# Kernel tuning notes

Hardware: AMD Instinct MI355X
Metric: run time of the kernel (lower is better)

## Reference

```python
import jax, jax.numpy as jnp
import numpy as np

N = 100000      # nodes
NT = 500000     # unique (s,o) pairs
R = 16          # original relations
RP = 16         # latent relations
EMB = 16
NUMCLS = 40


def setup_inputs() -> dict:
    key = jax.random.key(0)
    ks = jax.random.split(key, 10)
    s = jax.random.randint(ks[0], (NT,), 0, N)
    o = jax.random.randint(ks[1], (NT,), 0, N)
    rm = jnp.arange(RP)
    # faithful to source: oe = o*rm, se = s*rm (values in [0, N*RP))
    hrow = jnp.broadcast_to(s[None, :], (RP, NT)).reshape(-1).astype(jnp.int64)
    hcol = (o[None, :] * rm[:, None]).reshape(-1).astype(jnp.int64)
    vrow = (s[None, :] * rm[:, None]).reshape(-1).astype(jnp.int64)
    vcol = jnp.broadcast_to(o[None, :], (RP, NT)).reshape(-1).astype(jnp.int64)
    # multi-hot relation indicators per unique pair
    nhots = (jax.random.uniform(ks[2], (NT, R)) < 0.15).astype(jnp.float32)
    xav = lambda k, shp, fan: (jax.random.normal(k, shp, jnp.float32) * np.sqrt(2.0 / fan)).astype(jnp.float32)
    return {
        'nhots': nhots,
        'Wl1': xav(ks[3], (RP, R), R), 'bl1': jnp.zeros((RP,), jnp.float32),
        'Wl2': xav(ks[4], (RP, R), R), 'bl2': jnp.zeros((RP,), jnp.float32),
        'weights1': xav(ks[5], (RP, N, EMB), N),
        'weights2': xav(ks[6], (RP, EMB, NUMCLS), EMB),
        'bias1': jnp.zeros((EMB,), jnp.float32),
        'bias2': jnp.zeros((NUMCLS,), jnp.float32),
        'hrow': hrow, 'hcol': hcol, 'vrow': vrow, 'vcol': vcol,
    }


def reference(nhots, Wl1, bl1, Wl2, bl2, weights1, weights2, bias1, bias2,
              hrow, hcol, vrow, vcol):
    rp, n, e = weights1.shape
    nrp = n * rp
    # --- layer 1: softmax-gated latent relation values, column-normalized ---
    lat1 = jax.nn.softmax(nhots @ Wl1.T + bl1, axis=1)          # (nt, rp)
    vals1 = lat1.T.reshape(-1)                                   # (rp*nt,) rp-major, matches index order
    colsum = jax.ops.segment_sum(vals1, hcol, num_segments=nrp)
    vals1 = vals1 / colsum[hcol]
    # spmm: (n, n*rp) sparse  x  (n*rp, e) dense
    wflat = weights1.reshape(nrp, e)
    h = jax.ops.segment_sum(vals1[:, None] * wflat[hcol], hrow, num_segments=n)  # (n, e)
    h = jax.nn.relu(h + bias1)
    # --- layer 2: row-normalized ---
    lat2 = jax.nn.softmax(nhots @ Wl2.T + bl2, axis=1)
    vals2 = lat2.T.reshape(-1)
    rowsum = jax.ops.segment_sum(vals2, vrow, num_segments=nrp)
    vals2 = vals2 / rowsum[vrow]
    # spmm: (n*rp, n) sparse  x  (n, e) dense
    h2 = jax.ops.segment_sum(vals2[:, None] * h[vcol], vrow, num_segments=nrp)   # (n*rp, e)
    h2 = h2.reshape(rp, n, e)
    out = jnp.einsum('rhc,rnh->nc', weights2, h2) + bias2        # (n, numcls)
    return out
```

## Files before the change

kernel.cpp:

```cpp
#include <hip/hip_runtime.h>
#include <stdint.h>

#define NN 100000
#define NT 500000
#define RP 16
#define RR 16
#define EMB 16
#define NUMCLS 40
#define NRP (NN*RP)
#define MM (2*NN)
#define SCAN_BLOCKS ((MM + 255)/256)
#define NB16 6250

__global__ __launch_bounds__(256) void k_count(const int* __restrict__ s,
                                               const int* __restrict__ o,
                                               int* __restrict__ cnt){
    int t = blockIdx.x*256 + threadIdx.x;
    if (t >= NT) return;
    atomicAdd(&cnt[s[t]], 1);
    atomicAdd(&cnt[NN + o[t]], 1);
}

__global__ __launch_bounds__(256) void k_scan_blk(const int* __restrict__ cnt,
                                                  int* __restrict__ offs,
                                                  int* __restrict__ bsum){
    __shared__ int sm[256];
    int tid = threadIdx.x;
    int i = blockIdx.x*256 + tid;
    int v = (i < MM) ? cnt[i] : 0;
    sm[tid] = v; __syncthreads();
    for (int off = 1; off < 256; off <<= 1){
        int x = (tid >= off) ? sm[tid-off] : 0;
        __syncthreads();
        sm[tid] += x; __syncthreads();
    }
    if (i < MM) offs[i] = sm[tid] - v;
    if (tid == 255) bsum[blockIdx.x] = sm[255];
}

__global__ __launch_bounds__(1024) void k_scan_top(const int* __restrict__ bsum,
                                                   int* __restrict__ btot){
    __shared__ int sm[1024];
    int tid = threadIdx.x;
    int v = (tid < SCAN_BLOCKS) ? bsum[tid] : 0;
    sm[tid] = v; __syncthreads();
    for (int off = 1; off < 1024; off <<= 1){
        int x = (tid >= off) ? sm[tid-off] : 0;
        __syncthreads();
        sm[tid] += x; __syncthreads();
    }
    if (tid < SCAN_BLOCKS) btot[tid] = sm[tid] - v;
}

__global__ __launch_bounds__(256) void k_scan_add(int* __restrict__ offs,
                                                  const int* __restrict__ btot,
                                                  int* __restrict__ cur){
    int i = blockIdx.x*256 + threadIdx.x;
    if (i < MM){
        int v = offs[i] + btot[blockIdx.x];
        offs[i] = v;
        cur[i] = v;
    }
    if (i == 0) offs[MM] = 2*NT;
}

__global__ __launch_bounds__(256) void k_lat(
    const float* __restrict__ nhots,
    const float* __restrict__ Wl1, const float* __restrict__ bl1,
    const float* __restrict__ Wl2, const float* __restrict__ bl2,
    const int* __restrict__ srow, const int* __restrict__ ocol,
    int* __restrict__ cur,
    float* __restrict__ lat1q, float* __restrict__ lat2p,
    int* __restrict__ o_at_p, int* __restrict__ s_at_q)
{
    __shared__ float sW1[RP*RR], sW2[RP*RR], sb1[RP], sb2[RP];
    __shared__ float st1[256][17], st2[256][17];
    __shared__ int sq[256], sp[256];
    int tid = threadIdx.x;
    if (tid < RP*RR){ sW1[tid] = Wl1[tid]; sW2[tid] = Wl2[tid]; }
    if (tid < RP){ sb1[tid] = bl1[tid]; sb2[tid] = bl2[tid]; }
    __syncthreads();

    int t = blockIdx.x*256 + tid;
    int p = -1, q = -1;
    if (t < NT){
        int s_ = srow[t], o_ = ocol[t];
        p = atomicAdd(&cur[s_], 1);
        q = atomicAdd(&cur[NN + o_], 1) - NT;
        o_at_p[p] = o_;
        s_at_q[q] = s_;

        float nh[RR];
        const float4* npx = (const float4*)(nhots + (size_t)t * RR);
        #pragma unroll
        for (int u = 0; u < 4; u++){
            float4 v = npx[u];
            nh[4*u] = v.x; nh[4*u+1] = v.y; nh[4*u+2] = v.z; nh[4*u+3] = v.w;
        }
        float l1[RP], l2[RP];
        #pragma unroll
        for (int r = 0; r < RP; r++){
            float a = sb1[r], b = sb2[r];
            #pragma unroll
            for (int i = 0; i < RR; i++){ a += nh[i]*sW1[r*RR+i]; b += nh[i]*sW2[r*RR+i]; }
            l1[r] = a; l2[r] = b;
        }
        float m1 = l1[0], m2 = l2[0];
        #pragma unroll
        for (int r = 1; r < RP; r++){ m1 = fmaxf(m1, l1[r]); m2 = fmaxf(m2, l2[r]); }
        float s1 = 0.f, s2 = 0.f;
        #pragma unroll
        for (int r = 0; r < RP; r++){
            l1[r] = expf(l1[r]-m1); s1 += l1[r];
            l2[r] = expf(l2[r]-m2); s2 += l2[r];
        }
        float i1 = 1.f/s1, i2 = 1.f/s2;
        #pragma unroll
        for (int r = 0; r < RP; r++){ st1[tid][r] = l1[r]*i1; st2[tid][r] = l2[r]*i2; }
    }
    sq[tid] = q; sp[tid] = p;
    __syncthreads();

    int g = tid >> 4, e = tid & 15;
    #pragma unroll
    for (int k = 0; k < 16; k++){
        int ei = k*16 + g;
        int qq = sq[ei];
        if (qq >= 0){
            lat1q[(size_t)qq*16 + e] = st1[ei][e];
            lat2p[(size_t)sp[ei]*16 + e] = st2[ei][e];
        }
    }
}

__global__ __launch_bounds__(256) void k_CR(const int* __restrict__ offs,
                                            const float* __restrict__ lat1q,
                                            const float* __restrict__ lat2p,
                                            float* __restrict__ C,
                                            float* __restrict__ Rm,
                                            float* __restrict__ pbC,
                                            float* __restrict__ pbR){
    int gid = blockIdx.x*256 + threadIdx.x;
    int n = gid >> 4, e = gid & 15;
    float accC = 0.f, accR = 0.f;
    if (n < NN){
        int b = offs[NN+n] - NT, en = offs[NN+n+1] - NT;
        for (int i = b; i < en; i++) accC += lat1q[(size_t)i*16 + e];
        C[(size_t)n*16 + e] = accC;
        b = offs[n]; en = offs[n+1];
        for (int i = b; i < en; i++) accR += lat2p[(size_t)i*16 + e];
        Rm[(size_t)n*16 + e] = accR;
    }
    __shared__ float sa[16], sb[16];
    int g = threadIdx.x >> 4;
    if (e == 0){ sa[g] = accC; sb[g] = accR; }
    __syncthreads();
    if (threadIdx.x == 0){
        float a = 0.f, b = 0.f;
        #pragma unroll
        for (int k = 0; k < 16; k++){ a += sa[k]; b += sb[k]; }
        pbC[blockIdx.x] = a;
        pbR[blockIdx.x] = b;
    }
}

__global__ __launch_bounds__(1024) void k_red1(const float* __restrict__ pbC,
                                               const float* __restrict__ pbR,
                                               float* __restrict__ S0V){
    __shared__ float sa[1024], sb[1024];
    int tid = threadIdx.x;
    float a = 0.f, b = 0.f;
    for (int i = tid; i < NB16; i += 1024){ a += pbC[i]; b += pbR[i]; }
    sa[tid] = a; sb[tid] = b; __syncthreads();
    for (int off = 512; off > 0; off >>= 1){
        if (tid < off){ sa[tid] += sa[tid+off]; sb[tid] += sb[tid+off]; }
        __syncthreads();
    }
    if (tid == 0){ S0V[0] = sa[0]; S0V[1] = sb[0]; }
}

__global__ __launch_bounds__(256) void k_sums(const float* __restrict__ C,
                                              const float* __restrict__ Rm,
                                              const float* __restrict__ S0,
                                              float* __restrict__ invc,
                                              float* __restrict__ invr){
    int c = blockIdx.x*256 + threadIdx.x;
    if (c >= NRP) return;
    float a = 0.f, b = 0.f;
    if (c == 0){ a = S0[0]; b = S0[1]; }
    #pragma unroll
    for (int r = 1; r < RP; r++){
        int q = c / r;
        if (q*r == c && q < NN){
            a += C[(size_t)q*16 + r];
            b += Rm[(size_t)q*16 + r];
        }
    }
    invc[c] = (a > 0.f) ? 1.f/a : 0.f;
    invr[c] = (b > 0.f) ? 1.f/b : 0.f;
}

__global__ __launch_bounds__(256) void k_y(const int* __restrict__ offs,
                                           const float* __restrict__ lat1q,
                                           const int* __restrict__ s_at_q,
                                           const float* __restrict__ invc,
                                           const float* __restrict__ w1,
                                           float* __restrict__ hsum){
    int gid = blockIdx.x*256 + threadIdx.x;
    int o = gid >> 4, e = gid & 15;
    if (o >= NN) return;
    float Wb[RP];
    #pragma unroll
    for (int r = 0; r < RP; r++){
        size_t c = (size_t)o * r;
        Wb[r] = invc[c] * w1[c*16 + e];
    }
    int b = offs[NN+o] - NT, en = offs[NN+o+1] - NT;
    for (int i = b; i < en; i++){
        const float4* lp = (const float4*)(lat1q + (size_t)i*16);
        float4 v0 = lp[0], v1 = lp[1], v2 = lp[2], v3 = lp[3];
        float y = v0.x*Wb[0] + v0.y*Wb[1] + v0.z*Wb[2] + v0.w*Wb[3]
                + v1.x*Wb[4] + v1.y*Wb[5] + v1.z*Wb[6] + v1.w*Wb[7]
                + v2.x*Wb[8] + v2.y*Wb[9] + v2.z*Wb[10]+ v2.w*Wb[11]
                + v3.x*Wb[12]+ v3.y*Wb[13]+ v3.z*Wb[14]+ v3.w*Wb[15];
        int s = s_at_q[i];
        unsafeAtomicAdd(&hsum[(size_t)s*16 + e], y);
    }
}

__global__ __launch_bounds__(256) void k_P(const int* __restrict__ offs,
                                           const int* __restrict__ o_at_p,
                                           const float* __restrict__ lat2p,
                                           const float* __restrict__ hsum,
                                           const float* __restrict__ b1,
                                           float* __restrict__ P,
                                           float* __restrict__ pbV){
    int gid = blockIdx.x*256 + threadIdx.x;
    int n = gid >> 4, e = gid & 15;
    float be = b1[e];
    float acc[RP];
    #pragma unroll
    for (int r = 0; r < RP; r++) acc[r] = 0.f;
    if (n < NN){
        int b = offs[n], en = offs[n+1];
        for (int i = b; i < en; i++){
            int o = o_at_p[i];
            float hv = fmaxf(hsum[(size_t)o*16 + e] + be, 0.f);
            const float4* lp = (const float4*)(lat2p + (size_t)i*16);
            float4 v0 = lp[0], v1 = lp[1], v2 = lp[2], v3 = lp[3];
            acc[0] += v0.x*hv; acc[1] += v0.y*hv; acc[2] += v0.z*hv; acc[3] += v0.w*hv;
            acc[4] += v1.x*hv; acc[5] += v1.y*hv; acc[6] += v1.z*hv; acc[7] += v1.w*hv;
            acc[8] += v2.x*hv; acc[9] += v2.y*hv; acc[10]+= v2.z*hv; acc[11]+= v2.w*hv;
            acc[12]+= v3.x*hv; acc[13]+= v3.y*hv; acc[14]+= v3.z*hv; acc[15]+= v3.w*hv;
        }
        float* Pn = P + (size_t)n*240 + e;
        #pragma unroll
        for (int r = 1; r < RP; r++) Pn[(r-1)*16] = acc[r];
    }
    __shared__ float sm[256];
    sm[threadIdx.x] = acc[0]; __syncthreads();
    if (threadIdx.x < 16){
        float s = 0.f;
        #pragma unroll
        for (int k = 0; k < 16; k++) s += sm[k*16 + threadIdx.x];
        pbV[(size_t)blockIdx.x*16 + threadIdx.x] = s;
    }
}

__global__ __launch_bounds__(256) void k_red2(const float* __restrict__ pbV,
                                              float* __restrict__ S0V){
    int e = blockIdx.x;
    __shared__ float sm[256];
    int tid = threadIdx.x;
    float a = 0.f;
    for (int i = tid; i < NB16; i += 256) a += pbV[(size_t)i*16 + e];
    sm[tid] = a; __syncthreads();
    for (int off = 128; off > 0; off >>= 1){
        if (tid < off) sm[tid] += sm[tid+off];
        __syncthreads();
    }
    if (tid == 0) S0V[2 + e] = sm[0];
}

__global__ __launch_bounds__(256) void k_out(const float* __restrict__ P,
                                             const float* __restrict__ invr,
                                             const float* __restrict__ S0V,
                                             const float* __restrict__ w2,
                                             const float* __restrict__ b2,
                                             float* __restrict__ out){
    int n = blockIdx.x*256 + threadIdx.x;
    if (n >= NN) return;
    float acc[NUMCLS];
    #pragma unroll
    for (int cl = 0; cl < NUMCLS; cl++) acc[cl] = b2[cl];
    #pragma unroll 1
    for (int rr = 0; rr < RP; rr++){
        int c = rr*NN + n;
        float hrow[EMB];
        #pragma unroll
        for (int e = 0; e < EMB; e++) hrow[e] = 0.f;
        if (c == 0){
            #pragma unroll
            for (int e = 0; e < EMB; e++) hrow[e] = S0V[2 + e];
        }
        #pragma unroll
        for (int r = 1; r < RP; r++){
            int q = c / r;
            if (q*r == c && q < NN){
                const float* Pr = P + (size_t)q*240 + (r-1)*16;
                #pragma unroll
                for (int e = 0; e < EMB; e++) hrow[e] += Pr[e];
            }
        }
        float inv = invr[c];
        const float* wr = w2 + (size_t)rr*EMB*NUMCLS;
        #pragma unroll
        for (int e = 0; e < EMB; e++){
            float x = hrow[e] * inv;
            #pragma unroll
            for (int cl = 0; cl < NUMCLS; cl++) acc[cl] += x * wr[e*NUMCLS + cl];
        }
    }
    float4* op = (float4*)(out + (size_t)n*NUMCLS);
    #pragma unroll
    for (int q = 0; q < NUMCLS/4; q++)
        op[q] = make_float4(acc[4*q], acc[4*q+1], acc[4*q+2], acc[4*q+3]);
}

extern "C" void kernel_launch(void* const* d_in, const int* in_sizes, int n_in,
                              void* d_out, int out_size, void* d_ws, size_t ws_size,
                              hipStream_t stream)
{
    const float* nhots = (const float*)d_in[0];
    const float* Wl1   = (const float*)d_in[1];
    const float* bl1   = (const float*)d_in[2];
    const float* Wl2   = (const float*)d_in[3];
    const float* bl2   = (const float*)d_in[4];
    const float* w1    = (const float*)d_in[5];
    const float* w2    = (const float*)d_in[6];
    const float* b1    = (const float*)d_in[7];
    const float* b2    = (const float*)d_in[8];
    const int* srow = (const int*)d_in[9];
    const int* ocol = (const int*)d_in[12];

    float* base = (float*)d_ws;
    float* P     = base;
    float* lat1q = base;
    float* C     = base + (size_t)8000000;
    float* Rm    = base + (size_t)9600000;
    float* lat2p = base + (size_t)24000000;
    float* invc  = base + (size_t)32000000;
    float* invr  = base + (size_t)33600000;
    float* hsum  = base + (size_t)35200000;
    float* S0V   = base + (size_t)36800000;
    int*   cnt   = (int*)(base + (size_t)36800032);
    int*   cur   = cnt;
    int*   offs  = cnt + MM;
    int*   bsum  = offs + (MM+1);
    int*   btot  = bsum + 1024;
    int*   o_at_p = btot + 1024;
    int*   s_at_q = o_at_p + NT;
    float* pbC   = (float*)(s_at_q + NT);
    float* pbR   = pbC + NB16;
    float* pbV   = pbR + NB16;

    hipMemsetAsync(cnt, 0, (size_t)MM*4, stream);
    hipMemsetAsync(hsum, 0, (size_t)NN*16*4, stream);

    const int EB = (NT + 255)/256;
    const int CB = (NRP + 255)/256;
    const int NB = (NN + 255)/256;

    k_count   <<<EB, 256, 0, stream>>>(srow, ocol, cnt);
    k_scan_blk<<<SCAN_BLOCKS, 256, 0, stream>>>(cnt, offs, bsum);
    k_scan_top<<<1, 1024, 0, stream>>>(bsum, btot);
    k_scan_add<<<SCAN_BLOCKS, 256, 0, stream>>>(offs, btot, cur);
    k_lat     <<<EB, 256, 0, stream>>>(nhots, Wl1, bl1, Wl2, bl2, srow, ocol,
                                       cur, lat1q, lat2p, o_at_p, s_at_q);
    k_CR      <<<NB16, 256, 0, stream>>>(offs, lat1q, lat2p, C, Rm, pbC, pbR);
    k_red1    <<<1, 1024, 0, stream>>>(pbC, pbR, S0V);
    k_sums    <<<CB, 256, 0, stream>>>(C, Rm, S0V, invc, invr);
    k_y       <<<NB16, 256, 0, stream>>>(offs, lat1q, s_at_q, invc, w1, hsum);
    k_P       <<<NB16, 256, 0, stream>>>(offs, o_at_p, lat2p, hsum, b1, P, pbV);
    k_red2    <<<16, 256, 0, stream>>>(pbV, S0V);
    k_out     <<<NB, 256, 0, stream>>>(P, invr, S0V, w2, b2, (float*)d_out);
}
```

Baseline: 628.7 us.

## Scatter layer-2 partials into dense h2 buffer via atomics instead of divisor gather

k_P now atomically adds each per-relation partial into a dense (N*RP,16) buffer at row n*r, replacing the compact P array. k_out then reads one contiguous row per latent index instead of testing 15 divisors with integer division and gathering. This removes the divisor search and its divergent loads from k_out. In exchange it adds a roughly 100 MB memset, 15 scattered atomic adds per thread and a larger workspace that shifts the buffer offsets.

```diff
diff --git a/kernel.cpp b/kernel.cpp
--- a/kernel.cpp
+++ b/kernel.cpp
@@ -233,7 +233,7 @@
                                            const float* __restrict__ lat2p,
                                            const float* __restrict__ hsum,
                                            const float* __restrict__ b1,
-                                           float* __restrict__ P,
+                                           float* __restrict__ h2n,
                                            float* __restrict__ pbV){
     int gid = blockIdx.x*256 + threadIdx.x;
     int n = gid >> 4, e = gid & 15;
@@ -253,9 +253,10 @@
             acc[8] += v2.x*hv; acc[9] += v2.y*hv; acc[10]+= v2.z*hv; acc[11]+= v2.w*hv;
             acc[12]+= v3.x*hv; acc[13]+= v3.y*hv; acc[14]+= v3.z*hv; acc[15]+= v3.w*hv;
         }
-        float* Pn = P + (size_t)n*240 + e;
-        #pragma unroll
-        for (int r = 1; r < RP; r++) Pn[(r-1)*16] = acc[r];
+        #pragma unroll
+        for (int r = 1; r < RP; r++){
+            unsafeAtomicAdd(&h2n[(size_t)(n*r)*16 + e], acc[r]);
+        }
     }
     __shared__ float sm[256];
     sm[threadIdx.x] = acc[0]; __syncthreads();
@@ -282,7 +283,7 @@
     if (tid == 0) S0V[2 + e] = sm[0];
 }
 
-__global__ __launch_bounds__(256) void k_out(const float* __restrict__ P,
+__global__ __launch_bounds__(256) void k_out(const float* __restrict__ h2n,
                                              const float* __restrict__ invr,
                                              const float* __restrict__ S0V,
                                              const float* __restrict__ w2,
@@ -293,30 +294,25 @@
     float acc[NUMCLS];
     #pragma unroll
     for (int cl = 0; cl < NUMCLS; cl++) acc[cl] = b2[cl];
-    #pragma unroll 1
+    #pragma unroll 4
     for (int rr = 0; rr < RP; rr++){
         int c = rr*NN + n;
-        float hrow[EMB];
-        #pragma unroll
-        for (int e = 0; e < EMB; e++) hrow[e] = 0.f;
+        const float4* hp = (const float4*)(h2n + (size_t)c*16);
+        float4 h0 = hp[0], h1 = hp[1], h2 = hp[2], h3 = hp[3];
+        float inv = invr[c];
+        float hr[16];
+        hr[0]=h0.x;  hr[1]=h0.y;  hr[2]=h0.z;  hr[3]=h0.w;
+        hr[4]=h1.x;  hr[5]=h1.y;  hr[6]=h1.z;  hr[7]=h1.w;
+        hr[8]=h2.x;  hr[9]=h2.y;  hr[10]=h2.z; hr[11]=h2.w;
+        hr[12]=h3.x; hr[13]=h3.y; hr[14]=h3.z; hr[15]=h3.w;
         if (c == 0){
             #pragma unroll
-            for (int e = 0; e < EMB; e++) hrow[e] = S0V[2 + e];
-        }
-        #pragma unroll
-        for (int r = 1; r < RP; r++){
-            int q = c / r;
-            if (q*r == c && q < NN){
-                const float* Pr = P + (size_t)q*240 + (r-1)*16;
-                #pragma unroll
-                for (int e = 0; e < EMB; e++) hrow[e] += Pr[e];
-            }
-        }
-        float inv = invr[c];
+            for (int e = 0; e < EMB; e++) hr[e] += S0V[2+e];
+        }
         const float* wr = w2 + (size_t)rr*EMB*NUMCLS;
         #pragma unroll
         for (int e = 0; e < EMB; e++){
-            float x = hrow[e] * inv;
+            float x = hr[e] * inv;
             #pragma unroll
             for (int cl = 0; cl < NUMCLS; cl++) acc[cl] += x * wr[e*NUMCLS + cl];
         }
@@ -344,16 +340,16 @@
     const int* ocol = (const int*)d_in[12];
 
     float* base = (float*)d_ws;
-    float* P     = base;
+    float* h2n   = base;
     float* lat1q = base;
     float* C     = base + (size_t)8000000;
     float* Rm    = base + (size_t)9600000;
-    float* lat2p = base + (size_t)24000000;
-    float* invc  = base + (size_t)32000000;
-    float* invr  = base + (size_t)33600000;
-    float* hsum  = base + (size_t)35200000;
-    float* S0V   = base + (size_t)36800000;
-    int*   cnt   = (int*)(base + (size_t)36800032);
+    float* lat2p = base + (size_t)25600000;
+    float* invc  = base + (size_t)33600000;
+    float* invr  = base + (size_t)35200000;
+    float* hsum  = base + (size_t)36800000;
+    float* S0V   = base + (size_t)38400000;
+    int*   cnt   = (int*)(base + (size_t)38400032);
     int*   cur   = cnt;
     int*   offs  = cnt + MM;
     int*   bsum  = offs + (MM+1);
@@ -381,7 +377,8 @@
     k_red1    <<<1, 1024, 0, stream>>>(pbC, pbR, S0V);
     k_sums    <<<CB, 256, 0, stream>>>(C, Rm, S0V, invc, invr);
     k_y       <<<NB16, 256, 0, stream>>>(offs, lat1q, s_at_q, invc, w1, hsum);
-    k_P       <<<NB16, 256, 0, stream>>>(offs, o_at_p, lat2p, hsum, b1, P, pbV);
+    hipMemsetAsync(h2n, 0, (size_t)NRP*16*4, stream);
+    k_P       <<<NB16, 256, 0, stream>>>(offs, o_at_p, lat2p, hsum, b1, h2n, pbV);
     k_red2    <<<16, 256, 0, stream>>>(pbV, S0V);
-    k_out     <<<NB, 256, 0, stream>>>(P, invr, S0V, w2, b2, (float*)d_out);
-}
+    k_out     <<<NB, 256, 0, stream>>>(h2n, invr, S0V, w2, b2, (float*)d_out);
+}
```

Result: slower. 761.3 us (+21.1%).

## Split k_out relation loop across four wavefronts with shared-memory reduction

Applied to the files above, without the earlier changes.

The output kernel now assigns 64 nodes per block and gives each of the four wavefronts a quarter of the 16 latent relations, reducing partial class accumulators through LDS. This raises the number of blocks fourfold, increasing parallelism and latency hiding for the serial per-node relation loop. P rows are now read with float4 loads. Output is written through a coalesced shared-memory transpose instead of per-thread float4 strided stores. The cost is 42 KB of LDS per block, which may limit occupancy, plus a barrier.

```diff
diff --git a/kernel.cpp b/kernel.cpp
--- a/kernel.cpp
+++ b/kernel.cpp
@@ -288,43 +288,63 @@
                                              const float* __restrict__ w2,
                                              const float* __restrict__ b2,
                                              float* __restrict__ out){
-    int n = blockIdx.x*256 + threadIdx.x;
-    if (n >= NN) return;
+    __shared__ float sm[4][64][41];
+    int tid = threadIdx.x;
+    int w = tid >> 6;
+    int lane = tid & 63;
+    int n = blockIdx.x*64 + lane;
     float acc[NUMCLS];
     #pragma unroll
-    for (int cl = 0; cl < NUMCLS; cl++) acc[cl] = b2[cl];
-    #pragma unroll 1
-    for (int rr = 0; rr < RP; rr++){
-        int c = rr*NN + n;
-        float hrow[EMB];
-        #pragma unroll
-        for (int e = 0; e < EMB; e++) hrow[e] = 0.f;
-        if (c == 0){
+    for (int cl = 0; cl < NUMCLS; cl++) acc[cl] = 0.f;
+    if (n < NN){
+        #pragma unroll 1
+        for (int rw = 0; rw < 4; rw++){
+            int rr = w + rw*4;
+            int c = rr*NN + n;
+            float hrow[EMB];
             #pragma unroll
-            for (int e = 0; e < EMB; e++) hrow[e] = S0V[2 + e];
-        }
-        #pragma unroll
-        for (int r = 1; r < RP; r++){
-            int q = c / r;
-            if (q*r == c && q < NN){
-                const float* Pr = P + (size_t)q*240 + (r-1)*16;
+            for (int e = 0; e < EMB; e++) hrow[e] = 0.f;
+            if (c == 0){
                 #pragma unroll
-                for (int e = 0; e < EMB; e++) hrow[e] += Pr[e];
+                for (int e = 0; e < EMB; e++) hrow[e] = S0V[2+e];
             }
-        }
-        float inv = invr[c];
-        const float* wr = w2 + (size_t)rr*EMB*NUMCLS;
-        #pragma unroll
-        for (int e = 0; e < EMB; e++){
-            float x = hrow[e] * inv;
             #pragma unroll
-            for (int cl = 0; cl < NUMCLS; cl++) acc[cl] += x * wr[e*NUMCLS + cl];
-        }
-    }
-    float4* op = (float4*)(out + (size_t)n*NUMCLS);
-    #pragma unroll
-    for (int q = 0; q < NUMCLS/4; q++)
-        op[q] = make_float4(acc[4*q], acc[4*q+1], acc[4*q+2], acc[4*q+3]);
+            for (int r = 1; r < RP; r++){
+                int q = c / r;
+                if (q*r == c && q < NN){
+                    const float4* Pr = (const float4*)(P + (size_t)q*240 + (r-1)*16);
+                    float4 a0 = Pr[0], a1 = Pr[1], a2 = Pr[2], a3 = Pr[3];
+                    hrow[0]+=a0.x;  hrow[1]+=a0.y;  hrow[2]+=a0.z;  hrow[3]+=a0.w;
+                    hrow[4]+=a1.x;  hrow[5]+=a1.y;  hrow[6]+=a1.z;  hrow[7]+=a1.w;
+                    hrow[8]+=a2.x;  hrow[9]+=a2.y;  hrow[10]+=a2.z; hrow[11]+=a2.w;
+                    hrow[12]+=a3.x; hrow[13]+=a3.y; hrow[14]+=a3.z; hrow[15]+=a3.w;
+                }
+            }
+            float inv = invr[c];
+            const float* wr = w2 + (size_t)rr*EMB*NUMCLS;
+            #pragma unroll
+            for (int e = 0; e < EMB; e++){
+                float x = hrow[e] * inv;
+                #pragma unroll
+                for (int cl = 0; cl < NUMCLS; cl++) acc[cl] += x * wr[e*NUMCLS + cl];
+            }
+        }
+    }
+    #pragma unroll
+    for (int cl = 0; cl < NUMCLS; cl++) sm[w][lane][cl] = acc[cl];
+    __syncthreads();
+    int base_n = blockIdx.x*64;
+    #pragma unroll
+    for (int k = 0; k < 10; k++){
+        int f = k*256 + tid;
+        int nl = f / 40, cl = f - nl*40;
+        int nn = base_n + nl;
+        if (nn < NN){
+            float v = b2[cl] + sm[0][nl][cl] + sm[1][nl][cl]
+                             + sm[2][nl][cl] + sm[3][nl][cl];
+            out[(size_t)nn*NUMCLS + cl] = v;
+        }
+    }
 }
 
 extern "C" void kernel_launch(void* const* d_in, const int* in_sizes, int n_in,
@@ -369,7 +389,7 @@
 
     const int EB = (NT + 255)/256;
     const int CB = (NRP + 255)/256;
-    const int NB = (NN + 255)/256;
+    const int OB = (NN + 63)/64;
 
     k_count   <<<EB, 256, 0, stream>>>(srow, ocol, cnt);
     k_scan_blk<<<SCAN_BLOCKS, 256, 0, stream>>>(cnt, offs, bsum);
@@ -383,5 +403,5 @@
     k_y       <<<NB16, 256, 0, stream>>>(offs, lat1q, s_at_q, invc, w1, hsum);
     k_P       <<<NB16, 256, 0, stream>>>(offs, o_at_p, lat2p, hsum, b1, P, pbV);
     k_red2    <<<16, 256, 0, stream>>>(pbV, S0V);
-    k_out     <<<NB, 256, 0, stream>>>(P, invr, S0V, w2, b2, (float*)d_out);
-}
+    k_out     <<<OB, 256, 0, stream>>>(P, invr, S0V, w2, b2, (float*)d_out);
+}
```

After: 647.3 us. 1.03x slower.

## Parallelize output kernel over latent relations with shared-memory reduction and r-major P layout

Applied to the files above, without the earlier changes.

The P intermediate is stored relation-major ([r-1][n][e]) instead of node-major, so each latent-relation slice is contiguous and can be read with float4 loads. The output kernel now gives each thread one (relation, node) pair instead of looping over all 16 relations, and combines the per-relation partial class sums with shared-memory atomics before writing. This targets the low parallelism and serial relation loop of the old output kernel, which had only about 400 blocks. In exchange it adds shared atomics and a block sync, and relies on NN being divisible by 16.

```diff
diff --git a/kernel.cpp b/kernel.cpp
--- a/kernel.cpp
+++ b/kernel.cpp
@@ -233,7 +233,7 @@
                                            const float* __restrict__ lat2p,
                                            const float* __restrict__ hsum,
                                            const float* __restrict__ b1,
-                                           float* __restrict__ P,
+                                           float* __restrict__ Pr,
                                            float* __restrict__ pbV){
     int gid = blockIdx.x*256 + threadIdx.x;
     int n = gid >> 4, e = gid & 15;
@@ -253,9 +253,9 @@
             acc[8] += v2.x*hv; acc[9] += v2.y*hv; acc[10]+= v2.z*hv; acc[11]+= v2.w*hv;
             acc[12]+= v3.x*hv; acc[13]+= v3.y*hv; acc[14]+= v3.z*hv; acc[15]+= v3.w*hv;
         }
-        float* Pn = P + (size_t)n*240 + e;
-        #pragma unroll
-        for (int r = 1; r < RP; r++) Pn[(r-1)*16] = acc[r];
+        #pragma unroll
+        for (int r = 1; r < RP; r++)
+            Pr[((size_t)(r-1)*NN + n)*16 + e] = acc[r];
     }
     __shared__ float sm[256];
     sm[threadIdx.x] = acc[0]; __syncthreads();
@@ -282,49 +282,58 @@
     if (tid == 0) S0V[2 + e] = sm[0];
 }
 
-__global__ __launch_bounds__(256) void k_out(const float* __restrict__ P,
+__global__ __launch_bounds__(256) void k_out(const float* __restrict__ Pr,
                                              const float* __restrict__ invr,
                                              const float* __restrict__ S0V,
                                              const float* __restrict__ w2,
                                              const float* __restrict__ b2,
                                              float* __restrict__ out){
-    int n = blockIdx.x*256 + threadIdx.x;
-    if (n >= NN) return;
+    __shared__ float sm[16][41];
+    int tid = threadIdx.x;
+    int rr = tid >> 4, ni = tid & 15;
+    int n0 = blockIdx.x * 16;
+    int n = n0 + ni;
+    int c = rr*NN + n;
+    for (int k = tid; k < 16*41; k += 256) ((float*)sm)[k] = 0.f;
+    __syncthreads();
+
+    float hrow[EMB];
+    #pragma unroll
+    for (int e = 0; e < EMB; e++) hrow[e] = 0.f;
+    if (c == 0){
+        #pragma unroll
+        for (int e = 0; e < EMB; e++) hrow[e] = S0V[2+e];
+    }
+    #pragma unroll
+    for (int r = 1; r < RP; r++){
+        int q = c / r;
+        if (q*r == c && q < NN){
+            const float4* pp = (const float4*)(Pr + ((size_t)(r-1)*NN + q)*16);
+            float4 a0 = pp[0], a1 = pp[1], a2 = pp[2], a3 = pp[3];
+            hrow[0] += a0.x;  hrow[1] += a0.y;  hrow[2] += a0.z;  hrow[3] += a0.w;
+            hrow[4] += a1.x;  hrow[5] += a1.y;  hrow[6] += a1.z;  hrow[7] += a1.w;
+            hrow[8] += a2.x;  hrow[9] += a2.y;  hrow[10]+= a2.z;  hrow[11]+= a2.w;
+            hrow[12]+= a3.x;  hrow[13]+= a3.y;  hrow[14]+= a3.z;  hrow[15]+= a3.w;
+        }
+    }
+    float inv = invr[c];
     float acc[NUMCLS];
     #pragma unroll
-    for (int cl = 0; cl < NUMCLS; cl++) acc[cl] = b2[cl];
-    #pragma unroll 1
-    for (int rr = 0; rr < RP; rr++){
-        int c = rr*NN + n;
-        float hrow[EMB];
-        #pragma unroll
-        for (int e = 0; e < EMB; e++) hrow[e] = 0.f;
-        if (c == 0){
-            #pragma unroll
-            for (int e = 0; e < EMB; e++) hrow[e] = S0V[2 + e];
-        }
-        #pragma unroll
-        for (int r = 1; r < RP; r++){
-            int q = c / r;
-            if (q*r == c && q < NN){
-                const float* Pr = P + (size_t)q*240 + (r-1)*16;
-                #pragma unroll
-                for (int e = 0; e < EMB; e++) hrow[e] += Pr[e];
-            }
-        }
-        float inv = invr[c];
-        const float* wr = w2 + (size_t)rr*EMB*NUMCLS;
-        #pragma unroll
-        for (int e = 0; e < EMB; e++){
-            float x = hrow[e] * inv;
-            #pragma unroll
-            for (int cl = 0; cl < NUMCLS; cl++) acc[cl] += x * wr[e*NUMCLS + cl];
-        }
-    }
-    float4* op = (float4*)(out + (size_t)n*NUMCLS);
-    #pragma unroll
-    for (int q = 0; q < NUMCLS/4; q++)
-        op[q] = make_float4(acc[4*q], acc[4*q+1], acc[4*q+2], acc[4*q+3]);
+    for (int cl = 0; cl < NUMCLS; cl++) acc[cl] = 0.f;
+    const float* wr = w2 + (size_t)rr*EMB*NUMCLS;
+    #pragma unroll
+    for (int e = 0; e < EMB; e++){
+        float x = hrow[e] * inv;
+        #pragma unroll
+        for (int cl = 0; cl < NUMCLS; cl++) acc[cl] += x * wr[e*NUMCLS + cl];
+    }
+    #pragma unroll
+    for (int cl = 0; cl < NUMCLS; cl++) atomicAdd(&sm[ni][cl], acc[cl]);
+    __syncthreads();
+    for (int k = tid; k < 16*NUMCLS; k += 256){
+        int nl = k / NUMCLS, cl = k - nl*NUMCLS;
+        out[(size_t)(n0+nl)*NUMCLS + cl] = b2[cl] + sm[nl][cl];
+    }
 }
 
 extern "C" void kernel_launch(void* const* d_in, const int* in_sizes, int n_in,
@@ -344,7 +353,7 @@
     const int* ocol = (const int*)d_in[12];
 
     float* base = (float*)d_ws;
-    float* P     = base;
+    float* Pr    = base;
     float* lat1q = base;
     float* C     = base + (size_t)8000000;
     float* Rm    = base + (size_t)9600000;
@@ -369,7 +378,7 @@
 
     const int EB = (NT + 255)/256;
     const int CB = (NRP + 255)/256;
-    const int NB = (NN + 255)/256;
+    const int OB = NN/16;
 
     k_count   <<<EB, 256, 0, stream>>>(srow, ocol, cnt);
     k_scan_blk<<<SCAN_BLOCKS, 256, 0, stream>>>(cnt, offs, bsum);
@@ -381,7 +390,7 @@
     k_red1    <<<1, 1024, 0, stream>>>(pbC, pbR, S0V);
     k_sums    <<<CB, 256, 0, stream>>>(C, Rm, S0V, invc, invr);
     k_y       <<<NB16, 256, 0, stream>>>(offs, lat1q, s_at_q, invc, w1, hsum);
-    k_P       <<<NB16, 256, 0, stream>>>(offs, o_at_p, lat2p, hsum, b1, P, pbV);
+    k_P       <<<NB16, 256, 0, stream>>>(offs, o_at_p, lat2p, hsum, b1, Pr, pbV);
     k_red2    <<<16, 256, 0, stream>>>(pbV, S0V);
-    k_out     <<<NB, 256, 0, stream>>>(P, invr, S0V, w2, b2, (float*)d_out);
-}
+    k_out     <<<OB, 256, 0, stream>>>(Pr, invr, S0V, w2, b2, (float*)d_out);
+}
```

Result: slower. 926.1 us (+47.3%).
